# Kernel tuning notes

Measured on AMD Instinct MI355X. Metric: run time of the kernel, lower is better.

## Reference

```python
import jax, jax.numpy as jnp
import numpy as np

MUL = 32          # channel multiplicity of node features (32x0e + 32x1o)
N_SPEC = 4        # one-hot species dim (node_attrs = 4x0e)
N_EMB = 8         # radial (bessel) embedding dim
HID = 8           # invariant_neurons
TP_W = 4 * MUL    # tp.weight_numel: 4 'uvu' paths, 32 weights each
INV_SQRT3 = 0.5773502691896258


def setup_inputs() -> dict:
    key = jax.random.key(0)
    ks = jax.random.split(key, 13)
    N, E = 50000, 800000
    node_features = jax.random.normal(ks[0], (N, 4 * MUL), jnp.float32)
    node_attrs = jax.random.uniform(ks[1], (N, N_SPEC), dtype=jnp.float32)
    edge_index = jax.random.randint(ks[2], (2, E), 0, N)
    edge_attrs = jax.random.normal(ks[3], (E, 4), jnp.float32)          # SH: [0e | 1o(3)]
    edge_embedding = jax.random.uniform(ks[4], (E, N_EMB), dtype=jnp.float32)
    # learned parameters
    W1_s = jax.random.normal(ks[5], (MUL, MUL), jnp.float32)            # linear_1 scalar block
    W1_v = jax.random.normal(ks[6], (MUL, MUL), jnp.float32)            # linear_1 vector block
    fc_w1 = jax.random.normal(ks[7], (N_EMB, HID), jnp.float32)         # radial MLP layer 1
    fc_w2 = jax.random.normal(ks[8], (HID, TP_W), jnp.float32)          # radial MLP -> tp weights
    W2_s = jax.random.normal(ks[9], (2 * MUL, MUL), jnp.float32)        # linear_2: 64x0e -> 32x0e
    W2_v = jax.random.normal(ks[10], (2 * MUL, MUL), jnp.float32)       # linear_2: 64x1o -> 32x1o
    Wsc_s = jax.random.normal(ks[11], (MUL, N_SPEC, MUL), jnp.float32)  # sc: 0e x 0e -> 0e (uvw)
    Wsc_v = jax.random.normal(ks[12], (MUL, N_SPEC, MUL), jnp.float32)  # sc: 1o x 0e -> 1o (uvw)
    return dict(node_features=node_features, node_attrs=node_attrs,
                edge_attrs=edge_attrs, edge_embedding=edge_embedding,
                W1_s=W1_s, W1_v=W1_v, fc_w1=fc_w1, fc_w2=fc_w2,
                W2_s=W2_s, W2_v=W2_v, Wsc_s=Wsc_s, Wsc_v=Wsc_v,
                edge_index=edge_index)


def reference(node_features, node_attrs, edge_attrs, edge_embedding,
              W1_s, W1_v, fc_w1, fc_w2, W2_s, W2_v, Wsc_s, Wsc_v, edge_index):
    N = node_features.shape[0]
    edge_src = edge_index[1]
    edge_dst = edge_index[0]

    # split node features into scalar (32x0e) and vector (32x1o) blocks
    s = node_features[:, :MUL]                       # [N, 32]
    v = node_features[:, MUL:].reshape(N, MUL, 3)    # [N, 32, 3]

    # --- self-connection: FullyConnectedTensorProduct(features, node_attrs) ---
    sc_norm = 1.0 / jnp.sqrt(jnp.float32(MUL * N_SPEC))
    sc_s = jnp.einsum('nu,na,uaw->nw', s, node_attrs, Wsc_s) * sc_norm
    sc_v = jnp.einsum('nui,na,uaw->nwi', v, node_attrs, Wsc_v) * sc_norm

    # --- linear_1 (per-irrep linear, fan-in normalized) ---
    l1 = 1.0 / jnp.sqrt(jnp.float32(MUL))
    s1 = (s @ W1_s) * l1                                   # [N, 32]
    v1 = jnp.einsum('nui,uw->nwi', v, W1_v) * l1           # [N, 32, 3]

    # --- radial MLP: edge_embedding -> per-edge tp weights (silu) ---
    h = jax.nn.silu((edge_embedding @ fc_w1) / jnp.sqrt(jnp.float32(N_EMB)))
    w = (h @ fc_w2) / jnp.sqrt(jnp.float32(HID))           # [E, 128]
    w0, w1, w2, w3 = w[:, :MUL], w[:, MUL:2*MUL], w[:, 2*MUL:3*MUL], w[:, 3*MUL:]

    # --- gather source-node features per edge ---
    ss = s1[edge_src]                                      # [E, 32]
    vv = v1[edge_src]                                      # [E, 32, 3]
    a0 = edge_attrs[:, 0]                                  # [E]    0e SH
    a1 = edge_attrs[:, 1:4]                                # [E, 3] 1o SH

    # --- 'uvu' CG tensor product (4 paths) with per-edge weights ---
    o_s0 = w0 * ss * a0[:, None]                                    # 0e x 0e -> 0e
    o_s1 = w3 * jnp.einsum('eui,ei->eu', vv, a1) * INV_SQRT3        # 1o x 1o -> 0e
    o_v0 = w1[:, :, None] * ss[:, :, None] * a1[:, None, :]        # 0e x 1o -> 1o
    o_v1 = w2[:, :, None] * vv * a0[:, None, None]                 # 1o x 0e -> 1o

    eS = jnp.concatenate([o_s0, o_s1], axis=1)             # [E, 64] (64x0e)
    eV = jnp.concatenate([o_v0, o_v1], axis=1)             # [E, 64, 3] (64x1o)

    # --- scatter-add to destination nodes ---
    S = jax.ops.segment_sum(eS, edge_dst, num_segments=N)  # [N, 64]
    V = jax.ops.segment_sum(eV, edge_dst, num_segments=N)  # [N, 64, 3]

    # --- linear_2 (64x0e+64x1o -> 32x0e+32x1o) ---
    l2 = 1.0 / jnp.sqrt(jnp.float32(2 * MUL))
    s_out = (S @ W2_s) * l2
    v_out = jnp.einsum('nui,uw->nwi', V, W2_v) * l2

    # --- residual self-connection ---
    s_out = s_out + sc_s
    v_out = v_out + sc_v
    return jnp.concatenate([s_out, v_out.reshape(N, MUL * 3)], axis=1)  # [N, 128]
```

## Files before the change

### kernel.cpp

```cpp
#include <hip/hip_runtime.h>
#include <math.h>


typedef float  v2f __attribute__((ext_vector_type(2)));
typedef float  v4f __attribute__((ext_vector_type(4)));

__device__ __forceinline__ unsigned short f2bf(float x) {
    unsigned u = __float_as_uint(x);
    u += 0x7FFFu + ((u >> 16) & 1u);
    return (unsigned short)(u >> 16);
}
__device__ __forceinline__ float bf2f(unsigned short h) {
    return __uint_as_float(((unsigned)h) << 16);
}
__device__ __forceinline__ unsigned pack_bf(float lo, float hi) {
    unsigned ul = __float_as_uint(lo);
    ul = (ul + (0x7FFFu + ((ul >> 16) & 1u))) >> 16;
    unsigned uh = __float_as_uint(hi);
    uh = (uh + (0x7FFFu + ((uh >> 16) & 1u))) & 0xFFFF0000u;
    return ul | uh;
}
__device__ __forceinline__ float bf_lo(unsigned p) { return __uint_as_float(p << 16); }
__device__ __forceinline__ float bf_hi(unsigned p) { return __uint_as_float(p & 0xFFFF0000u); }

__global__ __launch_bounds__(256) void node_prep(
    const float* __restrict__ nf, const float* __restrict__ W1_s,
    const float* __restrict__ W1_v, const int* __restrict__ eidx,
    int* __restrict__ cnt, ushort* __restrict__ sv1, int N, int E)
{
    __shared__ float w1s[1024];
    __shared__ float w1v[1024];
    __shared__ float nrow[8][128];

    for (long long e = (long long)blockIdx.x * 256 + threadIdx.x; e < E;
         e += (long long)gridDim.x * 256)
        atomicAdd(cnt + eidx[(int)e], 1);

    int g = threadIdx.x >> 5;
    int w = threadIdx.x & 31;
    int n = blockIdx.x * 8 + g;

    for (int i = threadIdx.x; i < 1024; i += 256) {
        w1s[i] = W1_s[i];
        w1v[i] = W1_v[i];
    }
    if (n < N) {
        float4 q = *(const float4*)(nf + (size_t)n * 128 + w * 4);
        *(float4*)&nrow[g][w * 4] = q;
    }
    __syncthreads();
    if (n >= N) return;

    const float l1 = 0.17677669529663687f;
    const float* r = nrow[g];
    float ss = 0.f, vx = 0.f, vy = 0.f, vz = 0.f;
#pragma unroll 8
    for (int u = 0; u < 32; ++u) {
        float ws = w1s[u * 32 + w];
        float wv = w1v[u * 32 + w];
        ss += r[u] * ws;
        vx += r[32 + u * 3 + 0] * wv;
        vy += r[32 + u * 3 + 1] * wv;
        vz += r[32 + u * 3 + 2] * wv;
    }
    ushort4 o;
    o.x = f2bf(ss * l1); o.y = f2bf(vx * l1);
    o.z = f2bf(vy * l1); o.w = f2bf(vz * l1);
    *(ushort4*)(sv1 + (size_t)n * 128 + w * 4) = o;
}


__global__ __launch_bounds__(1024) void scan_a(
    const int* __restrict__ cnt, int* __restrict__ rs,
    int* __restrict__ bsum, int N)
{
    int i = blockIdx.x * 1024 + threadIdx.x;
    int lane = threadIdx.x & 63;
    int wid = threadIdx.x >> 6;
    int v = (i < N) ? cnt[i] : 0;
    int incl = v;
#pragma unroll
    for (int d = 1; d < 64; d <<= 1) {
        int t = __shfl_up(incl, d);
        if (lane >= d) incl += t;
    }
    __shared__ int wtot[16];
    __shared__ int woff[16];
    if (lane == 63) wtot[wid] = incl;
    __syncthreads();
    if (wid == 0) {
        int t = (lane < 16) ? wtot[lane] : 0;
        int s = t;
#pragma unroll
        for (int d = 1; d < 16; d <<= 1) {
            int q = __shfl_up(s, d);
            if (lane >= d) s += q;
        }
        if (lane < 16) woff[lane] = s - t;
        if (lane == 15) bsum[blockIdx.x] = s;
    }
    __syncthreads();
    if (i < N) rs[i] = woff[wid] + incl - v;
}

__global__ __launch_bounds__(64) void scan_b(
    const int* __restrict__ bsum, int* __restrict__ boff, int nb)
{
    int lane = threadIdx.x;
    int carry = 0;
    for (int base = 0; base < nb; base += 64) {
        int i = base + lane;
        int v = (i < nb) ? bsum[i] : 0;
        int s = v;
#pragma unroll
        for (int d = 1; d < 64; d <<= 1) {
            int t = __shfl_up(s, d);
            if (lane >= d) s += t;
        }
        if (i < nb) boff[i] = carry + s - v;
        carry += __shfl(s, 63);
    }
}

__global__ __launch_bounds__(256) void scatter_build(
    const float* __restrict__ ea, const float* __restrict__ ee,
    const float* __restrict__ fc1, const int* __restrict__ eidx,
    int* __restrict__ rs, const int* __restrict__ boff,
    ushort* __restrict__ hb, ushort* __restrict__ ab,
    int* __restrict__ srcb, int E)
{
    int e = blockIdx.x * 256 + threadIdx.x;
    if (e >= E) return;
    const float rs8 = 0.35355339059327373f;

    int d = eidx[e];
    int p = atomicAdd(rs + d, 1) + boff[d >> 10];

    const float* eep = ee + (size_t)e * 8;
    v4f e0 = *(const v4f*)eep;
    v4f e1 = *(const v4f*)(eep + 4);
    float ev[8] = {e0.x, e0.y, e0.z, e0.w, e1.x, e1.y, e1.z, e1.w};
    float hh[8];
#pragma unroll
    for (int k = 0; k < 8; ++k) {
        float t = 0.f;
#pragma unroll
        for (int i = 0; i < 8; ++i) t += ev[i] * fc1[i * 8 + k];
        t *= rs8;
        hh[k] = t * __builtin_amdgcn_rcpf(1.f + __expf(-t)) * rs8;
    }
    uint4 hp;
    hp.x = pack_bf(hh[0], hh[1]);
    hp.y = pack_bf(hh[2], hh[3]);
    hp.z = pack_bf(hh[4], hh[5]);
    hp.w = pack_bf(hh[6], hh[7]);
    *(uint4*)(hb + (size_t)p * 8) = hp;
    v4f a = *(const v4f*)(ea + (size_t)e * 4);
    uint2 ap;
    ap.x = pack_bf(a.x, a.y);
    ap.y = pack_bf(a.z, a.w);
    *(uint2*)(ab + (size_t)p * 4) = ap;
    srcb[p] = eidx[E + e];
}


__global__ __launch_bounds__(128) void reduce_kernel(
    const float* __restrict__ fc2, const ushort* __restrict__ sv1,
    const ushort* __restrict__ hb, const ushort* __restrict__ ab,
    const int* __restrict__ srcb, const int* __restrict__ rs_end,
    const int* __restrict__ boff, const int* __restrict__ cnt,
    ushort* __restrict__ SVb, int N)
{
    __shared__ float rec[2][64][20];

    int wv = threadIdx.x >> 6;
    int l  = threadIdx.x & 63;
    int h  = l >> 5;
    int u  = l & 31;
    int n = blockIdx.x * 2 + wv;
    if (n >= N) return;

    const float inv_sqrt3 = 0.5773502691896258f;

    v2f f01[8], f23[8];
#pragma unroll
    for (int k = 0; k < 8; ++k) {
        f01[k].x = fc2[k * 128 + u];
        f01[k].y = fc2[k * 128 + 32 + u];
        f23[k].x = fc2[k * 128 + 64 + u];
        f23[k].y = fc2[k * 128 + 96 + u];
    }

    int count = cnt[n];
    int start = rs_end[n] + boff[n >> 10] - count;

    float aS0 = 0.f, aS1 = 0.f;
    float aV0x = 0.f, aV0y = 0.f, aV0z = 0.f;
    float aV1x = 0.f, aV1y = 0.f, aV1z = 0.f;

    for (int j0 = 0; j0 < count; j0 += 64) {
        int nk = count - j0; if (nk > 64) nk = 64;
        if (l < nk) {
            size_t idx = (size_t)(start + j0 + l);
            uint4 hq = *(const uint4*)(hb + idx * 8);
            uint2 aq = *(const uint2*)(ab + idx * 4);
            int s = srcb[idx];
            float* rr = &rec[wv][l][0];
            *(v4f*)rr       = (v4f){bf_lo(hq.x), bf_hi(hq.x), bf_lo(hq.y), bf_hi(hq.y)};
            *(v4f*)(rr + 4) = (v4f){bf_lo(hq.z), bf_hi(hq.z), bf_lo(hq.w), bf_hi(hq.w)};
            *(v4f*)(rr + 8) = (v4f){bf_lo(aq.x), bf_hi(aq.x), bf_lo(aq.y), bf_hi(aq.y)};
            rr[12] = __int_as_float(s);
        }
        int pairs = (nk + 1) >> 1;
        int last = nk - 1;
        int s0 = __float_as_int(rec[wv][h <= last ? h : last][12]);
        ushort4 q = *(const ushort4*)(sv1 + (size_t)s0 * 128 + u * 4);
        for (int jj = 0; jj < pairs; ++jj) {
            int slot = jj * 2 + h;
            int nslot = slot + 2 <= last ? slot + 2 : last;
            int sN = __float_as_int(rec[wv][nslot][12]);
            ushort4 qn = *(const ushort4*)(sv1 + (size_t)sN * 128 + u * 4);

            float msk = (slot <= last) ? 1.f : 0.f;
            int slotc = slot <= last ? slot : last;
            const float* rr = &rec[wv][slotc][0];
            v4f H0 = *(const v4f*)rr;
            v4f H1 = *(const v4f*)(rr + 4);
            v4f A  = *(const v4f*)(rr + 8);
            float ss = bf2f(q.x) * msk;
            float vx = bf2f(q.y), vy = bf2f(q.z), vz = bf2f(q.w);

            v2f w01 = H0.x * f01[0] + H0.y * f01[1] + H0.z * f01[2] + H0.w * f01[3]
                    + H1.x * f01[4] + H1.y * f01[5] + H1.z * f01[6] + H1.w * f01[7];
            v2f w23 = H0.x * f23[0] + H0.y * f23[1] + H0.z * f23[2] + H0.w * f23[3]
                    + H1.x * f23[4] + H1.y * f23[5] + H1.z * f23[6] + H1.w * f23[7];

            float dv = (vx * A.y + vy * A.z + vz * A.w) * msk;
            aS0 += w01.x * (ss * A.x);
            aS1 += w23.y * dv;
            float c1 = w01.y * ss;
            aV0x += c1 * A.y; aV0y += c1 * A.z; aV0z += c1 * A.w;
            float c2 = w23.x * A.x * msk;
            aV1x += c2 * vx; aV1y += c2 * vy; aV1z += c2 * vz;
            q = qn;
        }
    }

    aS0  += __shfl_xor(aS0, 32);
    aS1  += __shfl_xor(aS1, 32);
    aV0x += __shfl_xor(aV0x, 32);
    aV0y += __shfl_xor(aV0y, 32);
    aV0z += __shfl_xor(aV0z, 32);
    aV1x += __shfl_xor(aV1x, 32);
    aV1y += __shfl_xor(aV1y, 32);
    aV1z += __shfl_xor(aV1z, 32);

    if (h == 0) {
        uint4 o;
        o.x = pack_bf(aS0, aS1 * inv_sqrt3);
        o.y = pack_bf(aV0x, aV0y);
        o.z = pack_bf(aV0z, aV1x);
        o.w = pack_bf(aV1y, aV1z);
        *(uint4*)(SVb + (size_t)n * 256 + u * 8) = o;
    }
}


__global__ __launch_bounds__(256) void node_final(
    const ushort* __restrict__ SVb, const float* __restrict__ W2_s,
    const float* __restrict__ W2_v, const float* __restrict__ nf,
    const float* __restrict__ nattr, const float* __restrict__ Wsc_s,
    const float* __restrict__ Wsc_v, float* __restrict__ out, int N)
{
    __shared__ float wq[4096];
    __shared__ float wsp[4096];
    __shared__ float wvp[4096];
    __shared__ float svt[8][8][32];
    __shared__ float nrow[8][128];

    int g = threadIdx.x >> 5;
    int w = threadIdx.x & 31;

    for (int i = threadIdx.x; i < 1024; i += 256) {
        int uu = i >> 5, ww = i & 31;
        *(float4*)&wq[i * 4] = make_float4(W2_s[i], W2_s[i + 1024],
                                           W2_v[i], W2_v[i + 1024]);
        const float* ps = Wsc_s + (size_t)uu * 128 + ww;
        const float* pv = Wsc_v + (size_t)uu * 128 + ww;
        *(float4*)&wsp[i * 4] = make_float4(ps[0], ps[32], ps[64], ps[96]);
        *(float4*)&wvp[i * 4] = make_float4(pv[0], pv[32], pv[64], pv[96]);
    }
    __syncthreads();

    const float l2 = 0.125f;
    const float sc_norm = 0.08838834764831843f;

    for (int t = 0; t < 4; ++t) {
        int n = blockIdx.x * 32 + g * 4 + t;
        if (n >= N) continue;
        uint4 p = *(const uint4*)(SVb + (size_t)n * 256 + w * 8);
        svt[g][0][w] = bf_lo(p.x); svt[g][1][w] = bf_hi(p.x);
        svt[g][2][w] = bf_lo(p.y); svt[g][3][w] = bf_hi(p.y);
        svt[g][4][w] = bf_lo(p.z); svt[g][5][w] = bf_hi(p.z);
        svt[g][6][w] = bf_lo(p.w); svt[g][7][w] = bf_hi(p.w);
        float4 q = *(const float4*)(nf + (size_t)n * 128 + w * 4);
        *(float4*)&nrow[g][w * 4] = q;
        float at0 = nattr[(size_t)n * 4 + 0];
        float at1 = nattr[(size_t)n * 4 + 1];
        float at2 = nattr[(size_t)n * 4 + 2];
        float at3 = nattr[(size_t)n * 4 + 3];

        float sa = 0.f, va0 = 0.f, va1 = 0.f, va2 = 0.f;
        float scs = 0.f, scv0 = 0.f, scv1 = 0.f, scv2 = 0.f;
#pragma unroll
        for (int u = 0; u < 32; ++u) {
            float4 qw = *(const float4*)&wq[(u * 32 + w) * 4];
            sa  += svt[g][0][u] * qw.x + svt[g][1][u] * qw.y;
            va0 += svt[g][2][u] * qw.z + svt[g][5][u] * qw.w;
            va1 += svt[g][3][u] * qw.z + svt[g][6][u] * qw.w;
            va2 += svt[g][4][u] * qw.z + svt[g][7][u] * qw.w;
            float4 ps = *(const float4*)&wsp[(u * 32 + w) * 4];
            float4 pv = *(const float4*)&wvp[(u * 32 + w) * 4];
            float cs = at0 * ps.x + at1 * ps.y + at2 * ps.z + at3 * ps.w;
            float cv = at0 * pv.x + at1 * pv.y + at2 * pv.z + at3 * pv.w;
            scs  += nrow[g][u] * cs;
            scv0 += nrow[g][32 + u * 3 + 0] * cv;
            scv1 += nrow[g][32 + u * 3 + 1] * cv;
            scv2 += nrow[g][32 + u * 3 + 2] * cv;
        }
        float* orow = out + (size_t)n * 128;
        orow[w] = sa * l2 + scs * sc_norm;
        orow[32 + w * 3 + 0] = va0 * l2 + scv0 * sc_norm;
        orow[32 + w * 3 + 1] = va1 * l2 + scv1 * sc_norm;
        orow[32 + w * 3 + 2] = va2 * l2 + scv2 * sc_norm;
    }
}


__global__ __launch_bounds__(256) void edge_kernel(
    const float* __restrict__ ea, const float* __restrict__ ee,
    const float* __restrict__ fc1, const float* __restrict__ fc2,
    const ushort* __restrict__ sv1, const int* __restrict__ eidx,
    float* __restrict__ SV, int E)
{
    long long tid = (long long)blockIdx.x * 256 + threadIdx.x;
    int e = (int)(tid >> 5);
    int u = (int)(tid & 31);
    if (e >= E) return;
    const float rs8 = 0.35355339059327373f;
    const float inv_sqrt3 = 0.5773502691896258f;
    float ev[8];
#pragma unroll
    for (int i = 0; i < 8; ++i) ev[i] = ee[(size_t)e * 8 + i];
    float h[8];
#pragma unroll
    for (int k = 0; k < 8; ++k) {
        float t = 0.f;
#pragma unroll
        for (int i = 0; i < 8; ++i) t += ev[i] * fc1[i * 8 + k];
        t *= rs8;
        h[k] = t / (1.f + expf(-t));
    }
    float w0 = 0.f, w1 = 0.f, w2 = 0.f, w3 = 0.f;
#pragma unroll
    for (int k = 0; k < 8; ++k) {
        const float* f2 = fc2 + k * 128;
        float hk = h[k];
        w0 += hk * f2[u];
        w1 += hk * f2[32 + u];
        w2 += hk * f2[64 + u];
        w3 += hk * f2[96 + u];
    }
    w0 *= rs8; w1 *= rs8; w2 *= rs8; w3 *= rs8;
    int dst = eidx[e];
    int src = eidx[E + e];
    float a0 = ea[(size_t)e * 4 + 0];
    float ax = ea[(size_t)e * 4 + 1];
    float ay = ea[(size_t)e * 4 + 2];
    float az = ea[(size_t)e * 4 + 3];
    ushort4 q = *(const ushort4*)(sv1 + (size_t)src * 128 + u * 4);
    float ss = bf2f(q.x), vx = bf2f(q.y), vy = bf2f(q.z), vz = bf2f(q.w);
    float dv = vx * ax + vy * ay + vz * az;
    float* o = SV + (size_t)dst * 256 + u * 8;
    atomicAdd(o + 0, w0 * ss * a0);
    atomicAdd(o + 1, w3 * dv * inv_sqrt3);
    float c1 = w1 * ss;
    atomicAdd(o + 2, c1 * ax);
    atomicAdd(o + 3, c1 * ay);
    atomicAdd(o + 4, c1 * az);
    float c2 = w2 * a0;
    atomicAdd(o + 5, c2 * vx);
    atomicAdd(o + 6, c2 * vy);
    atomicAdd(o + 7, c2 * vz);
}

__global__ __launch_bounds__(256) void node_final_f32(
    const float* __restrict__ SV, const float* __restrict__ W2_s,
    const float* __restrict__ W2_v, const float* __restrict__ nf,
    const float* __restrict__ nattr, const float* __restrict__ Wsc_s,
    const float* __restrict__ Wsc_v, float* __restrict__ out, int N)
{
    __shared__ float wq[4096];
    __shared__ float wsp[4096];
    __shared__ float wvp[4096];
    __shared__ float svt[8][8][32];
    __shared__ float nrow[8][128];

    int g = threadIdx.x >> 5;
    int w = threadIdx.x & 31;

    for (int i = threadIdx.x; i < 1024; i += 256) {
        int uu = i >> 5, ww = i & 31;
        *(float4*)&wq[i * 4] = make_float4(W2_s[i], W2_s[i + 1024],
                                           W2_v[i], W2_v[i + 1024]);
        const float* ps = Wsc_s + (size_t)uu * 128 + ww;
        const float* pv = Wsc_v + (size_t)uu * 128 + ww;
        *(float4*)&wsp[i * 4] = make_float4(ps[0], ps[32], ps[64], ps[96]);
        *(float4*)&wvp[i * 4] = make_float4(pv[0], pv[32], pv[64], pv[96]);
    }
    __syncthreads();

    const float l2 = 0.125f;
    const float sc_norm = 0.08838834764831843f;

    for (int t = 0; t < 4; ++t) {
        int n = blockIdx.x * 32 + g * 4 + t;
        if (n >= N) continue;
        const float* svp = SV + (size_t)n * 256 + w * 8;
        float4 p0 = *(const float4*)svp;
        float4 p1 = *(const float4*)(svp + 4);
        svt[g][0][w] = p0.x; svt[g][1][w] = p0.y;
        svt[g][2][w] = p0.z; svt[g][3][w] = p0.w;
        svt[g][4][w] = p1.x; svt[g][5][w] = p1.y;
        svt[g][6][w] = p1.z; svt[g][7][w] = p1.w;
        float4 q = *(const float4*)(nf + (size_t)n * 128 + w * 4);
        *(float4*)&nrow[g][w * 4] = q;
        float at0 = nattr[(size_t)n * 4 + 0];
        float at1 = nattr[(size_t)n * 4 + 1];
        float at2 = nattr[(size_t)n * 4 + 2];
        float at3 = nattr[(size_t)n * 4 + 3];

        float sa = 0.f, va0 = 0.f, va1 = 0.f, va2 = 0.f;
        float scs = 0.f, scv0 = 0.f, scv1 = 0.f, scv2 = 0.f;
#pragma unroll
        for (int u = 0; u < 32; ++u) {
            float4 qw = *(const float4*)&wq[(u * 32 + w) * 4];
            sa  += svt[g][0][u] * qw.x + svt[g][1][u] * qw.y;
            va0 += svt[g][2][u] * qw.z + svt[g][5][u] * qw.w;
            va1 += svt[g][3][u] * qw.z + svt[g][6][u] * qw.w;
            va2 += svt[g][4][u] * qw.z + svt[g][7][u] * qw.w;
            float4 ps = *(const float4*)&wsp[(u * 32 + w) * 4];
            float4 pv = *(const float4*)&wvp[(u * 32 + w) * 4];
            float cs = at0 * ps.x + at1 * ps.y + at2 * ps.z + at3 * ps.w;
            float cv = at0 * pv.x + at1 * pv.y + at2 * pv.z + at3 * pv.w;
            scs  += nrow[g][u] * cs;
            scv0 += nrow[g][32 + u * 3 + 0] * cv;
            scv1 += nrow[g][32 + u * 3 + 1] * cv;
            scv2 += nrow[g][32 + u * 3 + 2] * cv;
        }
        float* orow = out + (size_t)n * 128;
        orow[w] = sa * l2 + scs * sc_norm;
        orow[32 + w * 3 + 0] = va0 * l2 + scv0 * sc_norm;
        orow[32 + w * 3 + 1] = va1 * l2 + scv1 * sc_norm;
        orow[32 + w * 3 + 2] = va2 * l2 + scv2 * sc_norm;
    }
}

extern "C" void kernel_launch(void* const* d_in, const int* in_sizes, int n_in,
                              void* d_out, int out_size, void* d_ws, size_t ws_size,
                              hipStream_t stream) {
    const float* nf    = (const float*)d_in[0];
    const float* nattr = (const float*)d_in[1];
    const float* ea    = (const float*)d_in[2];
    const float* ee    = (const float*)d_in[3];
    const float* W1_s  = (const float*)d_in[4];
    const float* W1_v  = (const float*)d_in[5];
    const float* fc1   = (const float*)d_in[6];
    const float* fc2   = (const float*)d_in[7];
    const float* W2_s  = (const float*)d_in[8];
    const float* W2_v  = (const float*)d_in[9];
    const float* Wsc_s = (const float*)d_in[10];
    const float* Wsc_v = (const float*)d_in[11];
    const int*   eidx  = (const int*)d_in[12];

    int N = in_sizes[0] / 128;
    int E = in_sizes[12] / 2;

    float* ws = (float*)d_ws;
    ushort* sv1 = (ushort*)ws;
    ushort* SVb = (ushort*)(ws + (size_t)N * 64);
    ushort* hb  = (ushort*)(ws + (size_t)N * 192);
    ushort* ab  = (ushort*)(ws + (size_t)N * 192 + (size_t)E * 4);
    int* srcb = (int*)(ws + (size_t)N * 192 + (size_t)E * 6);
    int* cnt  = srcb + E;
    int* rs   = cnt + N;
    int* bsum = rs + N;
    int* boff = bsum + 64;

    size_t needed = ((size_t)N * 194 + (size_t)E * 7 + 128) * 4;

    int nb_node = (N + 7) / 8;
    int nbE = (E + 255) / 256;
    int nb_final = (N + 31) / 32;

    if (ws_size >= needed) {
        hipMemsetAsync(cnt, 0, (size_t)N * sizeof(int), stream);
        node_prep<<<nb_node, 256, 0, stream>>>(nf, W1_s, W1_v, eidx, cnt, sv1, N, E);
        int nbS = (N + 1023) / 1024;
        scan_a<<<nbS, 1024, 0, stream>>>(cnt, rs, bsum, N);
        scan_b<<<1, 64, 0, stream>>>(bsum, boff, nbS);
        scatter_build<<<nbE, 256, 0, stream>>>(ea, ee, fc1, eidx, rs, boff,
                                               hb, ab, srcb, E);
        int nbR = (N + 1) / 2;
        reduce_kernel<<<nbR, 128, 0, stream>>>(fc2, sv1, hb, ab, srcb,
                                               rs, boff, cnt, SVb, N);
        node_final<<<nb_final, 256, 0, stream>>>(SVb, W2_s, W2_v, nf, nattr,
                                                 Wsc_s, Wsc_v, (float*)d_out, N);
    } else {
        float* SVf = ws + (size_t)N * 64;
        int* cnt_f = (int*)(SVf + (size_t)N * 256);
        hipMemsetAsync(SVf, 0, (size_t)N * 256 * sizeof(float), stream);
        node_prep<<<nb_node, 256, 0, stream>>>(nf, W1_s, W1_v, eidx, cnt_f, sv1, N, E);
        long long tot = (long long)E * 32;
        int nb_edge = (int)((tot + 255) / 256);
        edge_kernel<<<nb_edge, 256, 0, stream>>>(ea, ee, fc1, fc2, sv1, eidx, SVf, E);
        node_final_f32<<<nb_final, 256, 0, stream>>>(SVf, W2_s, W2_v, nf, nattr,
                                                     Wsc_s, Wsc_v, (float*)d_out, N);
    }
}
```

Measured before the change: 237.9 us.

## Split scatter into permutation pass and record build; split final node kernel

The scatter step now first builds an edge permutation with atomics in a light kernel, then a second kernel walks positions in sorted order and writes the bf16 edge records contiguously, so record writes are coalesced instead of scattered. The final node kernel is split into a linear_2 kernel and a self-connection kernel that adds into the output. The aim is lower shared-memory use and higher occupancy in each final kernel, plus coalesced stores. In exchange it adds an extra E-sized perm buffer, two extra launches, gathered reads of edge inputs, and a read-modify-write of the output.

```diff
diff --git a/kernel.cpp b/kernel.cpp
--- a/kernel.cpp
+++ b/kernel.cpp
@@ -122,20 +122,29 @@
     }
 }
 
-__global__ __launch_bounds__(256) void scatter_build(
+__global__ __launch_bounds__(256) void scatter_kernel(
+    const int* __restrict__ eidx, int* __restrict__ rs,
+    const int* __restrict__ boff, int* __restrict__ perm, int E)
+{
+    int e = blockIdx.x * 256 + threadIdx.x;
+    if (e < E) {
+        int d = eidx[e];
+        int p = atomicAdd(rs + d, 1) + boff[d >> 10];
+        perm[p] = e;
+    }
+}
+
+__global__ __launch_bounds__(256) void build_records(
     const float* __restrict__ ea, const float* __restrict__ ee,
     const float* __restrict__ fc1, const int* __restrict__ eidx,
-    int* __restrict__ rs, const int* __restrict__ boff,
-    ushort* __restrict__ hb, ushort* __restrict__ ab,
-    int* __restrict__ srcb, int E)
-{
-    int e = blockIdx.x * 256 + threadIdx.x;
-    if (e >= E) return;
+    const int* __restrict__ perm, ushort* __restrict__ hb,
+    ushort* __restrict__ ab, int* __restrict__ srcb, int E)
+{
+    int p = blockIdx.x * 256 + threadIdx.x;
+    if (p >= E) return;
     const float rs8 = 0.35355339059327373f;
 
-    int d = eidx[e];
-    int p = atomicAdd(rs + d, 1) + boff[d >> 10];
-
+    int e = perm[p];
     const float* eep = ee + (size_t)e * 8;
     v4f e0 = *(const v4f*)eep;
     v4f e1 = *(const v4f*)(eep + 4);
@@ -266,34 +275,22 @@
 }
 
 
-__global__ __launch_bounds__(256) void node_final(
+__global__ __launch_bounds__(256) void final_linear(
     const ushort* __restrict__ SVb, const float* __restrict__ W2_s,
-    const float* __restrict__ W2_v, const float* __restrict__ nf,
-    const float* __restrict__ nattr, const float* __restrict__ Wsc_s,
-    const float* __restrict__ Wsc_v, float* __restrict__ out, int N)
+    const float* __restrict__ W2_v, float* __restrict__ out, int N)
 {
     __shared__ float wq[4096];
-    __shared__ float wsp[4096];
-    __shared__ float wvp[4096];
     __shared__ float svt[8][8][32];
-    __shared__ float nrow[8][128];
 
     int g = threadIdx.x >> 5;
     int w = threadIdx.x & 31;
 
-    for (int i = threadIdx.x; i < 1024; i += 256) {
-        int uu = i >> 5, ww = i & 31;
+    for (int i = threadIdx.x; i < 1024; i += 256)
         *(float4*)&wq[i * 4] = make_float4(W2_s[i], W2_s[i + 1024],
                                            W2_v[i], W2_v[i + 1024]);
-        const float* ps = Wsc_s + (size_t)uu * 128 + ww;
-        const float* pv = Wsc_v + (size_t)uu * 128 + ww;
-        *(float4*)&wsp[i * 4] = make_float4(ps[0], ps[32], ps[64], ps[96]);
-        *(float4*)&wvp[i * 4] = make_float4(pv[0], pv[32], pv[64], pv[96]);
-    }
     __syncthreads();
 
     const float l2 = 0.125f;
-    const float sc_norm = 0.08838834764831843f;
 
     for (int t = 0; t < 4; ++t) {
         int n = blockIdx.x * 32 + g * 4 + t;
@@ -303,6 +300,51 @@
         svt[g][2][w] = bf_lo(p.y); svt[g][3][w] = bf_hi(p.y);
         svt[g][4][w] = bf_lo(p.z); svt[g][5][w] = bf_hi(p.z);
         svt[g][6][w] = bf_lo(p.w); svt[g][7][w] = bf_hi(p.w);
+
+        float sa = 0.f, va0 = 0.f, va1 = 0.f, va2 = 0.f;
+#pragma unroll
+        for (int u = 0; u < 32; ++u) {
+            float4 qw = *(const float4*)&wq[(u * 32 + w) * 4];
+            sa  += svt[g][0][u] * qw.x + svt[g][1][u] * qw.y;
+            va0 += svt[g][2][u] * qw.z + svt[g][5][u] * qw.w;
+            va1 += svt[g][3][u] * qw.z + svt[g][6][u] * qw.w;
+            va2 += svt[g][4][u] * qw.z + svt[g][7][u] * qw.w;
+        }
+        float* orow = out + (size_t)n * 128;
+        orow[w] = sa * l2;
+        orow[32 + w * 3 + 0] = va0 * l2;
+        orow[32 + w * 3 + 1] = va1 * l2;
+        orow[32 + w * 3 + 2] = va2 * l2;
+    }
+}
+
+
+__global__ __launch_bounds__(256) void final_skip(
+    const float* __restrict__ nf, const float* __restrict__ nattr,
+    const float* __restrict__ Wsc_s, const float* __restrict__ Wsc_v,
+    float* __restrict__ out, int N)
+{
+    __shared__ v2f wsv2[4][1024];
+    __shared__ float nrow[8][128];
+
+    int g = threadIdx.x >> 5;
+    int w = threadIdx.x & 31;
+
+    for (int i = threadIdx.x; i < 1024; i += 256) {
+        int uu = i >> 5, ww = i & 31;
+        const float* ps = Wsc_s + (size_t)uu * 128 + ww;
+        const float* pv = Wsc_v + (size_t)uu * 128 + ww;
+#pragma unroll
+        for (int a = 0; a < 4; ++a)
+            wsv2[a][i] = (v2f){ps[a * 32], pv[a * 32]};
+    }
+    __syncthreads();
+
+    const float sc_norm = 0.08838834764831843f;
+
+    for (int t = 0; t < 4; ++t) {
+        int n = blockIdx.x * 32 + g * 4 + t;
+        if (n >= N) continue;
         float4 q = *(const float4*)(nf + (size_t)n * 128 + w * 4);
         *(float4*)&nrow[g][w * 4] = q;
         float at0 = nattr[(size_t)n * 4 + 0];
@@ -310,29 +352,22 @@
         float at2 = nattr[(size_t)n * 4 + 2];
         float at3 = nattr[(size_t)n * 4 + 3];
 
-        float sa = 0.f, va0 = 0.f, va1 = 0.f, va2 = 0.f;
         float scs = 0.f, scv0 = 0.f, scv1 = 0.f, scv2 = 0.f;
 #pragma unroll
         for (int u = 0; u < 32; ++u) {
-            float4 qw = *(const float4*)&wq[(u * 32 + w) * 4];
-            sa  += svt[g][0][u] * qw.x + svt[g][1][u] * qw.y;
-            va0 += svt[g][2][u] * qw.z + svt[g][5][u] * qw.w;
-            va1 += svt[g][3][u] * qw.z + svt[g][6][u] * qw.w;
-            va2 += svt[g][4][u] * qw.z + svt[g][7][u] * qw.w;
-            float4 ps = *(const float4*)&wsp[(u * 32 + w) * 4];
-            float4 pv = *(const float4*)&wvp[(u * 32 + w) * 4];
-            float cs = at0 * ps.x + at1 * ps.y + at2 * ps.z + at3 * ps.w;
-            float cv = at0 * pv.x + at1 * pv.y + at2 * pv.z + at3 * pv.w;
-            scs  += nrow[g][u] * cs;
-            scv0 += nrow[g][32 + u * 3 + 0] * cv;
-            scv1 += nrow[g][32 + u * 3 + 1] * cv;
-            scv2 += nrow[g][32 + u * 3 + 2] * cv;
+            int idx = u * 32 + w;
+            v2f csv = at0 * wsv2[0][idx] + at1 * wsv2[1][idx]
+                    + at2 * wsv2[2][idx] + at3 * wsv2[3][idx];
+            scs  += nrow[g][u] * csv.x;
+            scv0 += nrow[g][32 + u * 3 + 0] * csv.y;
+            scv1 += nrow[g][32 + u * 3 + 1] * csv.y;
+            scv2 += nrow[g][32 + u * 3 + 2] * csv.y;
         }
         float* orow = out + (size_t)n * 128;
-        orow[w] = sa * l2 + scs * sc_norm;
-        orow[32 + w * 3 + 0] = va0 * l2 + scv0 * sc_norm;
-        orow[32 + w * 3 + 1] = va1 * l2 + scv1 * sc_norm;
-        orow[32 + w * 3 + 2] = va2 * l2 + scv2 * sc_norm;
+        orow[w] += scs * sc_norm;
+        orow[32 + w * 3 + 0] += scv0 * sc_norm;
+        orow[32 + w * 3 + 1] += scv1 * sc_norm;
+        orow[32 + w * 3 + 2] += scv2 * sc_norm;
     }
 }
 
@@ -492,12 +527,13 @@
     ushort* hb  = (ushort*)(ws + (size_t)N * 192);
     ushort* ab  = (ushort*)(ws + (size_t)N * 192 + (size_t)E * 4);
     int* srcb = (int*)(ws + (size_t)N * 192 + (size_t)E * 6);
-    int* cnt  = srcb + E;
+    int* perm = srcb + E;
+    int* cnt  = perm + E;
     int* rs   = cnt + N;
     int* bsum = rs + N;
     int* boff = bsum + 64;
 
-    size_t needed = ((size_t)N * 194 + (size_t)E * 7 + 128) * 4;
+    size_t needed = ((size_t)N * 194 + (size_t)E * 8 + 128) * 4;
 
     int nb_node = (N + 7) / 8;
     int nbE = (E + 255) / 256;
@@ -509,13 +545,16 @@
         int nbS = (N + 1023) / 1024;
         scan_a<<<nbS, 1024, 0, stream>>>(cnt, rs, bsum, N);
         scan_b<<<1, 64, 0, stream>>>(bsum, boff, nbS);
-        scatter_build<<<nbE, 256, 0, stream>>>(ea, ee, fc1, eidx, rs, boff,
+        scatter_kernel<<<nbE, 256, 0, stream>>>(eidx, rs, boff, perm, E);
+        build_records<<<nbE, 256, 0, stream>>>(ea, ee, fc1, eidx, perm,
                                                hb, ab, srcb, E);
         int nbR = (N + 1) / 2;
         reduce_kernel<<<nbR, 128, 0, stream>>>(fc2, sv1, hb, ab, srcb,
                                                rs, boff, cnt, SVb, N);
-        node_final<<<nb_final, 256, 0, stream>>>(SVb, W2_s, W2_v, nf, nattr,
-                                                 Wsc_s, Wsc_v, (float*)d_out, N);
+        final_linear<<<nb_final, 256, 0, stream>>>(SVb, W2_s, W2_v,
+                                                   (float*)d_out, N);
+        final_skip<<<nb_final, 256, 0, stream>>>(nf, nattr, Wsc_s, Wsc_v,
+                                                 (float*)d_out, N);
     } else {
         float* SVf = ws + (size_t)N * 64;
         int* cnt_f = (int*)(SVf + (size_t)N * 256);
```

Result: slower. 282.3 us (+18.7%).

## Split edge scatter into permutation pass and coalesced record build; bf16 weights in node_final

Applied to the files above, without the earlier changes.

The edge bucketing kernel is split in two. A light scatter pass only does the atomic slot assignment and writes a permutation plus source index. A second pass then runs over destination-sorted positions, gathering edge inputs through the permutation and writing the hidden and SH records with coalesced stores instead of scattered ones. Separately, node_final stores its W2 and self-connection weights in shared memory as packed bf16, cutting LDS footprint and read traffic. This costs an extra launch, an extra permutation array, a random gather of the edge inputs, and lower precision on those weights.

```diff
diff --git a/kernel.cpp b/kernel.cpp
--- a/kernel.cpp
+++ b/kernel.cpp
@@ -122,20 +122,31 @@
     }
 }
 
-__global__ __launch_bounds__(256) void scatter_build(
+__global__ __launch_bounds__(256) void scatter_kernel(
+    const int* __restrict__ eidx, int* __restrict__ rs,
+    const int* __restrict__ boff, int* __restrict__ perm,
+    int* __restrict__ srcb, int E)
+{
+    int e = blockIdx.x * 256 + threadIdx.x;
+    if (e < E) {
+        int d = eidx[e];
+        int src = eidx[E + e];
+        int p = atomicAdd(rs + d, 1) + boff[d >> 10];
+        perm[p] = e;
+        srcb[p] = src;
+    }
+}
+
+__global__ __launch_bounds__(256) void build_records(
     const float* __restrict__ ea, const float* __restrict__ ee,
-    const float* __restrict__ fc1, const int* __restrict__ eidx,
-    int* __restrict__ rs, const int* __restrict__ boff,
-    ushort* __restrict__ hb, ushort* __restrict__ ab,
-    int* __restrict__ srcb, int E)
-{
-    int e = blockIdx.x * 256 + threadIdx.x;
-    if (e >= E) return;
+    const float* __restrict__ fc1, const int* __restrict__ perm,
+    ushort* __restrict__ hb, ushort* __restrict__ ab, int E)
+{
+    int p = blockIdx.x * 256 + threadIdx.x;
+    if (p >= E) return;
     const float rs8 = 0.35355339059327373f;
 
-    int d = eidx[e];
-    int p = atomicAdd(rs + d, 1) + boff[d >> 10];
-
+    int e = perm[p];
     const float* eep = ee + (size_t)e * 8;
     v4f e0 = *(const v4f*)eep;
     v4f e1 = *(const v4f*)(eep + 4);
@@ -160,7 +171,6 @@
     ap.x = pack_bf(a.x, a.y);
     ap.y = pack_bf(a.z, a.w);
     *(uint2*)(ab + (size_t)p * 4) = ap;
-    srcb[p] = eidx[E + e];
 }
 
 
@@ -272,9 +282,8 @@
     const float* __restrict__ nattr, const float* __restrict__ Wsc_s,
     const float* __restrict__ Wsc_v, float* __restrict__ out, int N)
 {
-    __shared__ float wq[4096];
-    __shared__ float wsp[4096];
-    __shared__ float wvp[4096];
+    __shared__ uint2 wqb[1024];
+    __shared__ uint4 wscb[1024];
     __shared__ float svt[8][8][32];
     __shared__ float nrow[8][128];
 
@@ -283,12 +292,12 @@
 
     for (int i = threadIdx.x; i < 1024; i += 256) {
         int uu = i >> 5, ww = i & 31;
-        *(float4*)&wq[i * 4] = make_float4(W2_s[i], W2_s[i + 1024],
-                                           W2_v[i], W2_v[i + 1024]);
+        wqb[i] = (uint2){pack_bf(W2_s[i], W2_s[i + 1024]),
+                         pack_bf(W2_v[i], W2_v[i + 1024])};
         const float* ps = Wsc_s + (size_t)uu * 128 + ww;
         const float* pv = Wsc_v + (size_t)uu * 128 + ww;
-        *(float4*)&wsp[i * 4] = make_float4(ps[0], ps[32], ps[64], ps[96]);
-        *(float4*)&wvp[i * 4] = make_float4(pv[0], pv[32], pv[64], pv[96]);
+        wscb[i] = (uint4){pack_bf(ps[0], ps[32]), pack_bf(ps[64], ps[96]),
+                          pack_bf(pv[0], pv[32]), pack_bf(pv[64], pv[96])};
     }
     __syncthreads();
 
@@ -314,15 +323,18 @@
         float scs = 0.f, scv0 = 0.f, scv1 = 0.f, scv2 = 0.f;
 #pragma unroll
         for (int u = 0; u < 32; ++u) {
-            float4 qw = *(const float4*)&wq[(u * 32 + w) * 4];
-            sa  += svt[g][0][u] * qw.x + svt[g][1][u] * qw.y;
-            va0 += svt[g][2][u] * qw.z + svt[g][5][u] * qw.w;
-            va1 += svt[g][3][u] * qw.z + svt[g][6][u] * qw.w;
-            va2 += svt[g][4][u] * qw.z + svt[g][7][u] * qw.w;
-            float4 ps = *(const float4*)&wsp[(u * 32 + w) * 4];
-            float4 pv = *(const float4*)&wvp[(u * 32 + w) * 4];
-            float cs = at0 * ps.x + at1 * ps.y + at2 * ps.z + at3 * ps.w;
-            float cv = at0 * pv.x + at1 * pv.y + at2 * pv.z + at3 * pv.w;
+            int idx = u * 32 + w;
+            uint2 qw = wqb[idx];
+            sa  += svt[g][0][u] * bf_lo(qw.x) + svt[g][1][u] * bf_hi(qw.x);
+            float w2va = bf_lo(qw.y), w2vb = bf_hi(qw.y);
+            va0 += svt[g][2][u] * w2va + svt[g][5][u] * w2vb;
+            va1 += svt[g][3][u] * w2va + svt[g][6][u] * w2vb;
+            va2 += svt[g][4][u] * w2va + svt[g][7][u] * w2vb;
+            uint4 wsc = wscb[idx];
+            float cs = at0 * bf_lo(wsc.x) + at1 * bf_hi(wsc.x)
+                     + at2 * bf_lo(wsc.y) + at3 * bf_hi(wsc.y);
+            float cv = at0 * bf_lo(wsc.z) + at1 * bf_hi(wsc.z)
+                     + at2 * bf_lo(wsc.w) + at3 * bf_hi(wsc.w);
             scs  += nrow[g][u] * cs;
             scv0 += nrow[g][32 + u * 3 + 0] * cv;
             scv1 += nrow[g][32 + u * 3 + 1] * cv;
@@ -492,12 +504,13 @@
     ushort* hb  = (ushort*)(ws + (size_t)N * 192);
     ushort* ab  = (ushort*)(ws + (size_t)N * 192 + (size_t)E * 4);
     int* srcb = (int*)(ws + (size_t)N * 192 + (size_t)E * 6);
-    int* cnt  = srcb + E;
+    int* perm = srcb + E;
+    int* cnt  = perm + E;
     int* rs   = cnt + N;
     int* bsum = rs + N;
     int* boff = bsum + 64;
 
-    size_t needed = ((size_t)N * 194 + (size_t)E * 7 + 128) * 4;
+    size_t needed = ((size_t)N * 194 + (size_t)E * 8 + 128) * 4;
 
     int nb_node = (N + 7) / 8;
     int nbE = (E + 255) / 256;
@@ -509,8 +522,8 @@
         int nbS = (N + 1023) / 1024;
         scan_a<<<nbS, 1024, 0, stream>>>(cnt, rs, bsum, N);
         scan_b<<<1, 64, 0, stream>>>(bsum, boff, nbS);
-        scatter_build<<<nbE, 256, 0, stream>>>(ea, ee, fc1, eidx, rs, boff,
-                                               hb, ab, srcb, E);
+        scatter_kernel<<<nbE, 256, 0, stream>>>(eidx, rs, boff, perm, srcb, E);
+        build_records<<<nbE, 256, 0, stream>>>(ea, ee, fc1, perm, hb, ab, E);
         int nbR = (N + 1) / 2;
         reduce_kernel<<<nbR, 128, 0, stream>>>(fc2, sv1, hb, ab, srcb,
                                                rs, boff, cnt, SVb, N);
```

Result: slower. 281.6 us (+18.4%).

## Pack per-edge records into one 32-byte struct and bf16-pack node_final weights

Applied to the files above, without the earlier changes.

Scatter_build now writes each edge's bf16 hidden activations, bf16 SH attributes and source index into a single 32-byte record instead of three separate arrays. The reduce kernel reads that record with two 16-byte loads instead of three scattered loads, trading 4 bytes of padding per edge for fewer memory transactions. Node_final stores the W2 and self-connection weights in LDS as packed bf16 pairs and uses v2f packed FMAs. This cuts LDS footprint and load count but lowers weight precision to bf16.

```diff
diff --git a/kernel.cpp b/kernel.cpp
--- a/kernel.cpp
+++ b/kernel.cpp
@@ -126,14 +126,14 @@
     const float* __restrict__ ea, const float* __restrict__ ee,
     const float* __restrict__ fc1, const int* __restrict__ eidx,
     int* __restrict__ rs, const int* __restrict__ boff,
-    ushort* __restrict__ hb, ushort* __restrict__ ab,
-    int* __restrict__ srcb, int E)
+    unsigned* __restrict__ recb, int E)
 {
     int e = blockIdx.x * 256 + threadIdx.x;
     if (e >= E) return;
     const float rs8 = 0.35355339059327373f;
 
     int d = eidx[e];
+    int src = eidx[E + e];
     int p = atomicAdd(rs + d, 1) + boff[d >> 10];
 
     const float* eep = ee + (size_t)e * 8;
@@ -154,20 +154,21 @@
     hp.y = pack_bf(hh[2], hh[3]);
     hp.z = pack_bf(hh[4], hh[5]);
     hp.w = pack_bf(hh[6], hh[7]);
-    *(uint4*)(hb + (size_t)p * 8) = hp;
     v4f a = *(const v4f*)(ea + (size_t)e * 4);
-    uint2 ap;
-    ap.x = pack_bf(a.x, a.y);
-    ap.y = pack_bf(a.z, a.w);
-    *(uint2*)(ab + (size_t)p * 4) = ap;
-    srcb[p] = eidx[E + e];
+    uint4 t2;
+    t2.x = pack_bf(a.x, a.y);
+    t2.y = pack_bf(a.z, a.w);
+    t2.z = (unsigned)src;
+    t2.w = 0u;
+    unsigned* rp = recb + (size_t)p * 8;
+    *(uint4*)rp       = hp;
+    *(uint4*)(rp + 4) = t2;
 }
 
 
 __global__ __launch_bounds__(128) void reduce_kernel(
     const float* __restrict__ fc2, const ushort* __restrict__ sv1,
-    const ushort* __restrict__ hb, const ushort* __restrict__ ab,
-    const int* __restrict__ srcb, const int* __restrict__ rs_end,
+    const unsigned* __restrict__ recb, const int* __restrict__ rs_end,
     const int* __restrict__ boff, const int* __restrict__ cnt,
     ushort* __restrict__ SVb, int N)
 {
@@ -201,15 +202,14 @@
     for (int j0 = 0; j0 < count; j0 += 64) {
         int nk = count - j0; if (nk > 64) nk = 64;
         if (l < nk) {
-            size_t idx = (size_t)(start + j0 + l);
-            uint4 hq = *(const uint4*)(hb + idx * 8);
-            uint2 aq = *(const uint2*)(ab + idx * 4);
-            int s = srcb[idx];
+            const unsigned* rp = recb + (size_t)(start + j0 + l) * 8;
+            uint4 hq = *(const uint4*)rp;
+            uint4 aq = *(const uint4*)(rp + 4);
             float* rr = &rec[wv][l][0];
             *(v4f*)rr       = (v4f){bf_lo(hq.x), bf_hi(hq.x), bf_lo(hq.y), bf_hi(hq.y)};
             *(v4f*)(rr + 4) = (v4f){bf_lo(hq.z), bf_hi(hq.z), bf_lo(hq.w), bf_hi(hq.w)};
             *(v4f*)(rr + 8) = (v4f){bf_lo(aq.x), bf_hi(aq.x), bf_lo(aq.y), bf_hi(aq.y)};
-            rr[12] = __int_as_float(s);
+            rr[12] = __uint_as_float(aq.z);
         }
         int pairs = (nk + 1) >> 1;
         int last = nk - 1;
@@ -272,10 +272,9 @@
     const float* __restrict__ nattr, const float* __restrict__ Wsc_s,
     const float* __restrict__ Wsc_v, float* __restrict__ out, int N)
 {
-    __shared__ float wq[4096];
-    __shared__ float wsp[4096];
-    __shared__ float wvp[4096];
-    __shared__ float svt[8][8][32];
+    __shared__ uint2 wqb[1024];
+    __shared__ uint4 wsvb[1024];
+    __shared__ v2f   svtp[8][32][4];
     __shared__ float nrow[8][128];
 
     int g = threadIdx.x >> 5;
@@ -283,12 +282,14 @@
 
     for (int i = threadIdx.x; i < 1024; i += 256) {
         int uu = i >> 5, ww = i & 31;
-        *(float4*)&wq[i * 4] = make_float4(W2_s[i], W2_s[i + 1024],
-                                           W2_v[i], W2_v[i + 1024]);
+        wqb[i] = (uint2){pack_bf(W2_s[i], W2_v[i]),
+                         pack_bf(W2_s[i + 1024], W2_v[i + 1024])};
         const float* ps = Wsc_s + (size_t)uu * 128 + ww;
         const float* pv = Wsc_v + (size_t)uu * 128 + ww;
-        *(float4*)&wsp[i * 4] = make_float4(ps[0], ps[32], ps[64], ps[96]);
-        *(float4*)&wvp[i * 4] = make_float4(pv[0], pv[32], pv[64], pv[96]);
+        wsvb[i] = (uint4){pack_bf(ps[0],  pv[0]),
+                          pack_bf(ps[32], pv[32]),
+                          pack_bf(ps[64], pv[64]),
+                          pack_bf(ps[96], pv[96])};
     }
     __syncthreads();
 
@@ -299,10 +300,10 @@
         int n = blockIdx.x * 32 + g * 4 + t;
         if (n >= N) continue;
         uint4 p = *(const uint4*)(SVb + (size_t)n * 256 + w * 8);
-        svt[g][0][w] = bf_lo(p.x); svt[g][1][w] = bf_hi(p.x);
-        svt[g][2][w] = bf_lo(p.y); svt[g][3][w] = bf_hi(p.y);
-        svt[g][4][w] = bf_lo(p.z); svt[g][5][w] = bf_hi(p.z);
-        svt[g][6][w] = bf_lo(p.w); svt[g][7][w] = bf_hi(p.w);
+        svtp[g][w][0] = (v2f){bf_lo(p.x), bf_lo(p.z)};
+        svtp[g][w][1] = (v2f){bf_hi(p.x), bf_hi(p.w)};
+        svtp[g][w][2] = (v2f){bf_lo(p.y), bf_hi(p.y)};
+        svtp[g][w][3] = (v2f){bf_hi(p.z), bf_lo(p.w)};
         float4 q = *(const float4*)(nf + (size_t)n * 128 + w * 4);
         *(float4*)&nrow[g][w * 4] = q;
         float at0 = nattr[(size_t)n * 4 + 0];
@@ -310,29 +311,40 @@
         float at2 = nattr[(size_t)n * 4 + 2];
         float at3 = nattr[(size_t)n * 4 + 3];
 
-        float sa = 0.f, va0 = 0.f, va1 = 0.f, va2 = 0.f;
-        float scs = 0.f, scv0 = 0.f, scv1 = 0.f, scv2 = 0.f;
+        v2f sa_va2 = (v2f){0.f, 0.f};
+        v2f va01   = (v2f){0.f, 0.f};
+        v2f scv01  = (v2f){0.f, 0.f};
+        float scs = 0.f, scv2 = 0.f;
 #pragma unroll
         for (int u = 0; u < 32; ++u) {
-            float4 qw = *(const float4*)&wq[(u * 32 + w) * 4];
-            sa  += svt[g][0][u] * qw.x + svt[g][1][u] * qw.y;
-            va0 += svt[g][2][u] * qw.z + svt[g][5][u] * qw.w;
-            va1 += svt[g][3][u] * qw.z + svt[g][6][u] * qw.w;
-            va2 += svt[g][4][u] * qw.z + svt[g][7][u] * qw.w;
-            float4 ps = *(const float4*)&wsp[(u * 32 + w) * 4];
-            float4 pv = *(const float4*)&wvp[(u * 32 + w) * 4];
-            float cs = at0 * ps.x + at1 * ps.y + at2 * ps.z + at3 * ps.w;
-            float cv = at0 * pv.x + at1 * pv.y + at2 * pv.z + at3 * pv.w;
-            scs  += nrow[g][u] * cs;
-            scv0 += nrow[g][32 + u * 3 + 0] * cv;
-            scv1 += nrow[g][32 + u * 3 + 1] * cv;
-            scv2 += nrow[g][32 + u * 3 + 2] * cv;
+            int idx = u * 32 + w;
+            uint2 qw = wqb[idx];
+            float w2s_a = bf_lo(qw.x), w2v_a = bf_hi(qw.x);
+            float w2s_b = bf_lo(qw.y), w2v_b = bf_hi(qw.y);
+            v2f Q0 = svtp[g][u][0], Q1 = svtp[g][u][1];
+            v2f Q2 = svtp[g][u][2], Q3 = svtp[g][u][3];
+            sa_va2 += Q0 * (v2f){w2s_a, w2v_a};
+            sa_va2 += Q1 * (v2f){w2s_b, w2v_b};
+            va01   += Q2 * (v2f){w2v_a, w2v_a};
+            va01   += Q3 * (v2f){w2v_b, w2v_b};
+            uint4 wv = wsvb[idx];
+            v2f csv = at0 * (v2f){bf_lo(wv.x), bf_hi(wv.x)}
+                    + at1 * (v2f){bf_lo(wv.y), bf_hi(wv.y)}
+                    + at2 * (v2f){bf_lo(wv.z), bf_hi(wv.z)}
+                    + at3 * (v2f){bf_lo(wv.w), bf_hi(wv.w)};
+            float su = nrow[g][u];
+            float vx = nrow[g][32 + u * 3 + 0];
+            float vy = nrow[g][32 + u * 3 + 1];
+            float vz = nrow[g][32 + u * 3 + 2];
+            scs   += su * csv.x;
+            scv01 += (v2f){vx, vy} * (v2f){csv.y, csv.y};
+            scv2  += vz * csv.y;
         }
         float* orow = out + (size_t)n * 128;
-        orow[w] = sa * l2 + scs * sc_norm;
-        orow[32 + w * 3 + 0] = va0 * l2 + scv0 * sc_norm;
-        orow[32 + w * 3 + 1] = va1 * l2 + scv1 * sc_norm;
-        orow[32 + w * 3 + 2] = va2 * l2 + scv2 * sc_norm;
+        orow[w]              = sa_va2.x * l2 + scs     * sc_norm;
+        orow[32 + w * 3 + 0] = va01.x   * l2 + scv01.x * sc_norm;
+        orow[32 + w * 3 + 1] = va01.y   * l2 + scv01.y * sc_norm;
+        orow[32 + w * 3 + 2] = sa_va2.y * l2 + scv2    * sc_norm;
     }
 }
 
@@ -489,15 +501,13 @@
     float* ws = (float*)d_ws;
     ushort* sv1 = (ushort*)ws;
     ushort* SVb = (ushort*)(ws + (size_t)N * 64);
-    ushort* hb  = (ushort*)(ws + (size_t)N * 192);
-    ushort* ab  = (ushort*)(ws + (size_t)N * 192 + (size_t)E * 4);
-    int* srcb = (int*)(ws + (size_t)N * 192 + (size_t)E * 6);
-    int* cnt  = srcb + E;
+    unsigned* recb = (unsigned*)(ws + (size_t)N * 192);
+    int* cnt  = (int*)(ws + (size_t)N * 192 + (size_t)E * 8);
     int* rs   = cnt + N;
     int* bsum = rs + N;
     int* boff = bsum + 64;
 
-    size_t needed = ((size_t)N * 194 + (size_t)E * 7 + 128) * 4;
+    size_t needed = ((size_t)N * 194 + (size_t)E * 8 + 128) * 4;
 
     int nb_node = (N + 7) / 8;
     int nbE = (E + 255) / 256;
@@ -510,10 +520,10 @@
         scan_a<<<nbS, 1024, 0, stream>>>(cnt, rs, bsum, N);
         scan_b<<<1, 64, 0, stream>>>(bsum, boff, nbS);
         scatter_build<<<nbE, 256, 0, stream>>>(ea, ee, fc1, eidx, rs, boff,
-                                               hb, ab, srcb, E);
+                                               recb, E);
         int nbR = (N + 1) / 2;
-        reduce_kernel<<<nbR, 128, 0, stream>>>(fc2, sv1, hb, ab, srcb,
-                                               rs, boff, cnt, SVb, N);
+        reduce_kernel<<<nbR, 128, 0, stream>>>(fc2, sv1, recb, rs, boff, cnt,
+                                               SVb, N);
         node_final<<<nb_final, 256, 0, stream>>>(SVb, W2_s, W2_v, nf, nattr,
                                                  Wsc_s, Wsc_v, (float*)d_out, N);
     } else {
```

Result: faster. 218.6 us (-8.1%).
